# Performance work log

Hardware: AMD Instinct MI355X
Metric: run time of the kernel (lower is better)

## Reference

```python
import jax, jax.numpy as jnp
import numpy as np

L_XYZ = 10  # fourier freqs for position -> 3 + 6*10 = 63 dims
L_DIR = 4   # fourier freqs for direction -> 3 + 6*4 = 27 dims
DIM = 32    # radiance feature dim per depth layer
PPP = 4     # points (depth layers) per pixel
HID = 128   # MLP hidden width
UCH = 64    # UNet hidden channels


def pe(x, L):
    # fourier positional encoding: [x, sin(2^k x), cos(2^k x)]
    f = (2.0 ** jnp.arange(L)).astype(x.dtype)
    xf = x[..., None] * f  # [..., 3, L]
    s = jnp.sin(xf).reshape(x.shape[:-1] + (-1,))
    c = jnp.cos(xf).reshape(x.shape[:-1] + (-1,))
    return jnp.concatenate([x, s, c], axis=-1)


def conv(x, w, b):
    y = jax.lax.conv_general_dilated(x, w, (1, 1), 'SAME',
                                     dimension_numbers=('NCHW', 'OIHW', 'NCHW'))
    return y + b[None, :, None, None]


def setup_inputs() -> dict:
    key = jax.random.key(0)
    ks = jax.random.split(key, 24)
    H = W = 384
    zbufs = jax.random.uniform(ks[0], (H, W, PPP), dtype=jnp.float32)  # depths in [0,1)
    o = jax.random.normal(ks[1], (H, W, 3), dtype=jnp.float32)
    d = jax.random.normal(ks[2], (H, W, 3), dtype=jnp.float32)
    d = d / jnp.linalg.norm(d, axis=-1, keepdims=True)
    cos = jax.random.uniform(ks[3], (H, W, 1), dtype=jnp.float32) * 0.5 + 0.5
    ray = jnp.concatenate([o, d, cos], axis=-1)  # [H,W,7]
    gt = jax.random.uniform(ks[4], (H, W, 3), dtype=jnp.float32)
    mask_gt = jnp.ones((H, W, 1), dtype=jnp.float32)
    xyz_o = jax.random.normal(ks[5], (1024, 3), dtype=jnp.float32)
    in_xyz = 3 + 6 * L_XYZ
    in_dir = 3 + 6 * L_DIR
    in_ch = DIM * PPP
    p = {}
    p['w1'] = jax.random.normal(ks[6], (in_xyz, HID), dtype=jnp.float32) * 0.05
    p['b1'] = jnp.zeros((HID,), dtype=jnp.float32)
    p['w2'] = jax.random.normal(ks[7], (HID, HID), dtype=jnp.float32) * 0.05
    p['b2'] = jnp.zeros((HID,), dtype=jnp.float32)
    p['w3'] = jax.random.normal(ks[8], (HID + in_dir, DIM), dtype=jnp.float32) * 0.05
    p['b3'] = jnp.zeros((DIM,), dtype=jnp.float32)
    p['mpn_w1'] = jax.random.normal(ks[9], (in_ch, in_ch, 3, 3), dtype=jnp.float32) * 0.02
    p['mpn_b1'] = jnp.zeros((in_ch,), dtype=jnp.float32)
    p['mpn_w2'] = jax.random.normal(ks[10], (in_ch, in_ch, 3, 3), dtype=jnp.float32) * 0.02
    p['mpn_b2'] = jnp.zeros((in_ch,), dtype=jnp.float32)
    p['uw1'] = jax.random.normal(ks[11], (UCH, in_ch, 3, 3), dtype=jnp.float32) * 0.02
    p['ub1'] = jnp.zeros((UCH,), dtype=jnp.float32)
    p['uw2'] = jax.random.normal(ks[12], (UCH, UCH, 3, 3), dtype=jnp.float32) * 0.02
    p['ub2'] = jnp.zeros((UCH,), dtype=jnp.float32)
    p['uw3'] = jax.random.normal(ks[13], (3, UCH, 3, 3), dtype=jnp.float32) * 0.02
    p['ub3'] = jnp.zeros((3,), dtype=jnp.float32)
    inp = {'zbufs': zbufs, 'ray': ray, 'gt': gt, 'mask_gt': mask_gt,
           'isTrain': 1, 'xyz_o': xyz_o}
    inp.update(p)
    return inp


def reference(zbufs, ray, gt, mask_gt, isTrain, xyz_o,
              w1, b1, w2, b2, w3, b3,
              mpn_w1, mpn_b1, mpn_w2, mpn_b2,
              uw1, ub1, uw2, ub2, uw3, ub3):
    H, W, P = zbufs.shape
    o = ray[..., :3]
    dirs = ray[..., 3:6]
    cos = ray[..., 6:7]
    thresh = 0.2 if isTrain else 0.0
    # dense equivalent of boolean-mask gather -> MLP -> scatter into zeros
    mask = (zbufs > thresh).astype(zbufs.dtype)  # [H,W,P]
    # xyz_near = o + dirs * zbuf / cos  (xyznear path)
    xyz = o[..., None, :] + dirs[..., None, :] * zbufs[..., None] / cos[..., None]  # [H,W,P,3]
    x = pe(xyz, L_XYZ)                                   # [H,W,P,63]
    h = jax.nn.relu(x @ w1 + b1)                         # [H,W,P,HID]
    h = jax.nn.relu(h @ w2 + b2)
    dpe = pe(dirs, L_DIR)                                # [H,W,27]
    dpe = jnp.broadcast_to(dpe[..., None, :], h.shape[:-1] + (dpe.shape[-1],))
    feat = jnp.concatenate([h, dpe], axis=-1) @ w3 + b3  # [H,W,P,DIM]
    feat = feat * mask[..., None]                        # zeros where pix_mask is False
    # per-layer permute(2,3,0,1) + cat(dim=1) == [1, P*DIM, H, W]
    rdmp = feat.transpose(2, 3, 0, 1).reshape(1, P * DIM, H, W)
    # MPN: predicted per-channel mask
    m = jax.nn.sigmoid(conv(jax.nn.relu(conv(rdmp, mpn_w1, mpn_b1)), mpn_w2, mpn_b2))
    fuse = rdmp * m
    fea_map = jax.nn.sigmoid(fuse[0, :3].transpose(1, 2, 0))  # [H,W,3]
    # UNet refinement to RGB
    u = jax.nn.relu(conv(fuse, uw1, ub1))
    u = jax.nn.relu(conv(u, uw2, ub2))
    img = jax.nn.sigmoid(conv(u, uw3, ub3))[0].transpose(1, 2, 0)  # [H,W,3]
    return img
```

## Files before the change

kernel.cpp:

```cpp
#include <hip/hip_runtime.h>
#include <hip/hip_bf16.h>
#include <math.h>

typedef __attribute__((ext_vector_type(8))) unsigned short ushort8;
typedef __attribute__((ext_vector_type(8))) __bf16 bf16x8;
typedef __attribute__((ext_vector_type(4))) float floatx4;

constexpr int IMGW = 384;
constexpr int NPIX = IMGW * IMGW;

__device__ __forceinline__ unsigned short f2bf(float f) {
  union { float f; unsigned u; } v; v.f = f;
  unsigned u = v.u;
  return (unsigned short)((u + 0x7fffu + ((u >> 16) & 1u)) >> 16);
}
__device__ __forceinline__ float bf2f(unsigned short h) {
  union { unsigned u; float f; } v; v.u = ((unsigned)h) << 16; return v.f;
}
__device__ __forceinline__ unsigned pk2bf(float a, float b) {
  float2 f2; f2.x = a; f2.y = b;
  __hip_bfloat162 h = __float22bfloat162_rn(f2);
  union { __hip_bfloat162 h; unsigned u; } u; u.h = h; return u.u;
}
__device__ __forceinline__ floatx4 mfma16(bf16x8 a, bf16x8 b, floatx4 c) {
  return __builtin_amdgcn_mfma_f32_16x16x32_bf16(a, b, c, 0, 0, 0);
}
__device__ __forceinline__ bf16x8 lds_frag(const unsigned short* p) {
  return *reinterpret_cast<const bf16x8*>(p);
}
__device__ __forceinline__ bf16x8 u4_to_bf(uint4 v) {
  union { uint4 u; bf16x8 b; } c; c.u = v; return c.b;
}

__device__ __forceinline__ void convB_elem(const float* __restrict__ w,
                                           unsigned short* __restrict__ wt,
                                           int i, int CIN, int G, int NT) {
  int j = i & 7, lane = (i >> 3) & 63;
  int rest = i >> 9;
  int nt = rest % NT; int rest2 = rest / NT;
  int g = rest2 % G;  int ks = rest2 / G;
  int q = lane >> 4, m = lane & 15;
  int co = (g * NT + nt) * 16 + m;
  int k = ks * 32 + q * 8 + j;
  int nb = k / CIN, ci = k - nb * CIN;
  wt[i] = f2bf(w[(co * CIN + ci) * 9 + nb]);
}

__global__ __launch_bounds__(256) void prep_all(
    const float* __restrict__ w1, const float* __restrict__ w2, const float* __restrict__ w3,
    const float* __restrict__ mw1, const float* __restrict__ mw2,
    const float* __restrict__ uw1, const float* __restrict__ uw2,
    unsigned short* __restrict__ w1A, unsigned short* __restrict__ w2A,
    unsigned short* __restrict__ w3A,
    unsigned short* __restrict__ cw1, unsigned short* __restrict__ cw2,
    unsigned short* __restrict__ cu1, unsigned short* __restrict__ cu2) {
  int i = blockIdx.x * 256 + threadIdx.x;
  if (i < 28672) {
    if (i < 8192) {
      int j = i & 7, lane = (i >> 3) & 63, t = i >> 9;
      int mt = t >> 1, ks = t & 1;
      int ch_out = mt * 16 + (lane & 15);
      int kp = ks * 32 + (lane >> 4) * 8 + j;
      int chunk = kp >> 3, sl = kp & 7;
      float val;
      if (chunk == 7 && sl >= 4) {
        int c = sl - 4;
        val = (c < 3) ? w1[c * 128 + ch_out] : 0.0f;
      } else {
        const int coordA[8] = {0,0,0,1,1,2,2,2};
        const int octA[8]   = {0,4,8,2,6,0,4,8};
        const int coordB[8] = {0,0,1,1,1,2,2,2};
        const int octB[8]   = {2,6,0,4,8,2,6,0};
        int rc  = (sl < 4) ? coordA[chunk] : coordB[chunk];
        int oct = ((sl < 4) ? octA[chunk] : octB[chunk]) + ((sl >> 1) & 1);
        int korig = ((sl & 1) ? 33 : 3) + rc * 10 + oct;
        val = w1[korig * 128 + ch_out];
      }
      w1A[i] = f2bf(val);
    } else if (i < 24576) {
      int i2 = i - 8192;
      int j = i2 & 7, lane = (i2 >> 3) & 63, t = i2 >> 9;
      int mt = t >> 2, ks = t & 3;
      int ch_out = mt * 16 + (lane & 15);
      int kp = ks * 32 + (lane >> 4) * 8 + j;
      int c_orig = ((kp >> 2) & 7) * 16 + (kp >> 5) * 4 + (kp & 3);
      w2A[i2] = f2bf(w2[c_orig * 128 + ch_out]);
    } else {
      int i3 = i - 24576;
      int j = i3 & 7, lane = (i3 >> 3) & 63, t = i3 >> 9;
      int mt = t >> 2, ks = t & 3;
      int ch_out = mt * 16 + (lane & 15);
      int kp = ks * 32 + (lane >> 4) * 8 + j;
      int c_orig = ((kp >> 2) & 7) * 16 + (kp >> 5) * 4 + (kp & 3);
      w3A[i3] = f2bf(w3[c_orig * 32 + ch_out]);
    }
    return;
  }
  i -= 28672;
  if (i < 147456) { convB_elem(mw1, cw1, i, 128, 4, 2); return; }
  i -= 147456;
  if (i < 147456) { convB_elem(mw2, cw2, i, 128, 4, 2); return; }
  i -= 147456;
  if (i < 73728)  { convB_elem(uw1, cu1, i, 128, 4, 1); return; }
  i -= 73728;
  if (i < 36864)  { convB_elem(uw2, cu2, i, 64, 4, 1); return; }
}

__global__ __launch_bounds__(256) void dcon_kernel(
    const float* __restrict__ ray, const float* __restrict__ w3,
    const float* __restrict__ b3, float* __restrict__ dconG) {
  __shared__ float dpe[8][28];
  int tid = threadIdx.x;
  int pl = tid >> 5, c = tid & 31;
  int pixel = blockIdx.x * 8 + pl;
  const float* r = ray + (size_t)pixel * 7;
  if (c < 3) dpe[pl][c] = r[3 + c];
  if (c < 12) {
    int cc = c >> 2, f = c & 3;
    float s, co;
    __sincosf(r[3 + cc] * (float)(1 << f), &s, &co);
    dpe[pl][3 + cc * 4 + f]  = s;
    dpe[pl][15 + cc * 4 + f] = co;
  }
  __syncthreads();
  float acc = b3[c];
  #pragma unroll
  for (int d = 0; d < 27; ++d)
    acc += dpe[pl][d] * w3[(128 + d) * 32 + c];
  dconG[(size_t)pixel * 32 + c] = acc;
}

__global__ __launch_bounds__(64, 3) void mlp_kernel(
    const float* __restrict__ zbufs, const float* __restrict__ ray,
    const int* __restrict__ isTrain,
    const float* __restrict__ b1, const float* __restrict__ b2,
    const unsigned short* __restrict__ w1A, const unsigned short* __restrict__ w2A,
    const unsigned short* __restrict__ w3A, const float* __restrict__ dconG,
    unsigned short* __restrict__ rdmp, int blk0) {
  __shared__ __align__(16) unsigned short H[64 * 136];

  const int blk = blk0 + blockIdx.x;
  const int lane = threadIdx.x;
  const int q = lane >> 4, m = lane & 15;
  const float thresh = (isTrain[0] != 0) ? 0.2f : 0.0f;

  float fA[2], fB[2];
  int cAi[2], cBi[2];
  #pragma unroll
  for (int half = 0; half < 2; ++half) {
    int ch = half * 4 + q;
    cAi[half] = (ch <= 2) ? 0 : ((ch <= 4) ? 1 : 2);
    fA[half]  = (ch == 0 || ch == 5) ? 1.0f :
                (ch == 1 || ch == 6) ? 16.0f :
                (ch == 2 || ch == 7) ? 256.0f :
                (ch == 3) ? 4.0f : 64.0f;
    cBi[half] = (ch <= 1) ? 0 : ((ch <= 4) ? 1 : 2);
    fB[half]  = (ch == 2) ? 1.0f :
                (ch == 0 || ch == 5) ? 4.0f :
                (ch == 3) ? 16.0f :
                (ch == 1 || ch == 6) ? 64.0f : 256.0f;
  }

  bf16x8 bx[4][2];
  float zs[4];
  #pragma unroll
  for (int nt = 0; nt < 4; ++nt) {
    int s = nt * 16 + m;
    int sg = blk * 64 + s;
    int pixel = sg >> 2;
    float z = zbufs[sg];
    zs[nt] = z;
    const float* r = ray + (size_t)pixel * 7;
    float t = z / r[6];
    float xv0 = r[0] + r[3] * t, xv1 = r[1] + r[4] * t, xv2 = r[2] + r[5] * t;
    #pragma unroll
    for (int half = 0; half < 2; ++half) {
      float uA = (cAi[half] == 0) ? xv0 : ((cAi[half] == 1) ? xv1 : xv2);
      float uB = (cBi[half] == 0) ? xv0 : ((cBi[half] == 1) ? xv1 : xv2);
      float sa, ca, sb, cb;
      __sincosf(uA * fA[half], &sa, &ca);
      __sincosf(uB * fB[half], &sb, &cb);
      float t2a = sa + sa;
      float sa1 = t2a * ca, ca1 = fmaf(-t2a, sa, 1.0f);
      float t2b = sb + sb;
      float sb1 = t2b * cb, cb1 = fmaf(-t2b, sb, 1.0f);
      if (half == 1 && q == 3) { sb = xv0; cb = xv1; sb1 = xv2; cb1 = 0.0f; }
      uint4 dv;
      dv.x = pk2bf(sa, ca); dv.y = pk2bf(sa1, ca1);
      dv.z = pk2bf(sb, cb); dv.w = pk2bf(sb1, cb1);
      bx[nt][half] = u4_to_bf(dv);
    }
  }

  #pragma unroll 1
  for (int half = 0; half < 2; ++half) {
    floatx4 acc[4][4];
    #pragma unroll
    for (int mt = 0; mt < 4; ++mt) {
      float4 bb = *reinterpret_cast<const float4*>(b1 + (half * 4 + mt) * 16 + q * 4);
      #pragma unroll
      for (int nt = 0; nt < 4; ++nt) {
        acc[mt][nt][0] = bb.x; acc[mt][nt][1] = bb.y;
        acc[mt][nt][2] = bb.z; acc[mt][nt][3] = bb.w;
      }
    }
    #pragma unroll
    for (int ks = 0; ks < 2; ++ks) {
      #pragma unroll
      for (int mt = 0; mt < 4; ++mt) {
        int mtg = half * 4 + mt;
        bf16x8 a = *reinterpret_cast<const bf16x8*>(w1A + (((mtg << 1) + ks) << 9) + lane * 8);
        #pragma unroll
        for (int nt = 0; nt < 4; ++nt)
          acc[mt][nt] = mfma16(a, bx[nt][ks], acc[mt][nt]);
      }
    }
    #pragma unroll
    for (int nt = 0; nt < 4; ++nt) {
      uint4* base = reinterpret_cast<uint4*>(&H[(nt * 16 + m) * 136 + q * 32 + half * 16]);
      #pragma unroll
      for (int g = 0; g < 2; ++g) {
        uint4 v;
        v.x = pk2bf(fmaxf(acc[2*g][nt][0], 0.0f),   fmaxf(acc[2*g][nt][1], 0.0f));
        v.y = pk2bf(fmaxf(acc[2*g][nt][2], 0.0f),   fmaxf(acc[2*g][nt][3], 0.0f));
        v.z = pk2bf(fmaxf(acc[2*g+1][nt][0], 0.0f), fmaxf(acc[2*g+1][nt][1], 0.0f));
        v.w = pk2bf(fmaxf(acc[2*g+1][nt][2], 0.0f), fmaxf(acc[2*g+1][nt][3], 0.0f));
        base[g] = v;
      }
    }
  }

  {
    uint4 keep[4][2];
    #pragma unroll 1
    for (int half = 0; half < 2; ++half) {
      floatx4 acc[4][4];
      #pragma unroll
      for (int mt = 0; mt < 4; ++mt) {
        float4 bb = *reinterpret_cast<const float4*>(b2 + (half * 4 + mt) * 16 + q * 4);
        #pragma unroll
        for (int nt = 0; nt < 4; ++nt) {
          acc[mt][nt][0] = bb.x; acc[mt][nt][1] = bb.y;
          acc[mt][nt][2] = bb.z; acc[mt][nt][3] = bb.w;
        }
      }
      bf16x8 acur[4], anxt[4];
      #pragma unroll
      for (int mt = 0; mt < 4; ++mt)
        acur[mt] = *reinterpret_cast<const bf16x8*>(
            w2A + ((((half * 4 + mt) << 2) + 0) << 9) + lane * 8);
      #pragma unroll 1
      for (int ks = 0; ks < 4; ++ks) {
        if (ks + 1 < 4) {
          #pragma unroll
          for (int mt = 0; mt < 4; ++mt)
            anxt[mt] = *reinterpret_cast<const bf16x8*>(
                w2A + ((((half * 4 + mt) << 2) + ks + 1) << 9) + lane * 8);
        }
        bf16x8 bf[4];
        #pragma unroll
        for (int nt = 0; nt < 4; ++nt)
          bf[nt] = lds_frag(H + (nt * 16 + m) * 136 + ks * 32 + q * 8);
        #pragma unroll
        for (int mt = 0; mt < 4; ++mt)
          #pragma unroll
          for (int nt = 0; nt < 4; ++nt)
            acc[mt][nt] = mfma16(acur[mt], bf[nt], acc[mt][nt]);
        #pragma unroll
        for (int mt = 0; mt < 4; ++mt) acur[mt] = anxt[mt];
      }
      #pragma unroll
      for (int nt = 0; nt < 4; ++nt) {
        #pragma unroll
        for (int g = 0; g < 2; ++g) {
          uint4 v;
          v.x = pk2bf(fmaxf(acc[2*g][nt][0], 0.0f),   fmaxf(acc[2*g][nt][1], 0.0f));
          v.y = pk2bf(fmaxf(acc[2*g][nt][2], 0.0f),   fmaxf(acc[2*g][nt][3], 0.0f));
          v.z = pk2bf(fmaxf(acc[2*g+1][nt][0], 0.0f), fmaxf(acc[2*g+1][nt][1], 0.0f));
          v.w = pk2bf(fmaxf(acc[2*g+1][nt][2], 0.0f), fmaxf(acc[2*g+1][nt][3], 0.0f));
          if (half == 0) {
            keep[nt][g] = v;
          } else {
            *reinterpret_cast<uint4*>(&H[(nt * 16 + m) * 136 + q * 32 + 16 + g * 8]) = v;
          }
        }
      }
    }
    #pragma unroll
    for (int nt = 0; nt < 4; ++nt)
      #pragma unroll
      for (int g = 0; g < 2; ++g)
        *reinterpret_cast<uint4*>(&H[(nt * 16 + m) * 136 + q * 32 + g * 8]) = keep[nt][g];
  }

  {
    floatx4 acc[2][4];
    const float* dg = dconG + (size_t)blk * 512;
    #pragma unroll
    for (int nt = 0; nt < 4; ++nt) {
      int s = nt * 16 + m;
      #pragma unroll
      for (int mt = 0; mt < 2; ++mt)
        acc[mt][nt] = *reinterpret_cast<const floatx4*>(dg + (s >> 2) * 32 + mt * 16 + q * 4);
    }
    #pragma unroll
    for (int ks = 0; ks < 4; ++ks) {
      bf16x8 bf[4];
      #pragma unroll
      for (int nt = 0; nt < 4; ++nt)
        bf[nt] = lds_frag(H + (nt * 16 + m) * 136 + ks * 32 + q * 8);
      #pragma unroll
      for (int mt = 0; mt < 2; ++mt) {
        bf16x8 a = *reinterpret_cast<const bf16x8*>(w3A + (((mt << 2) + ks) << 9) + lane * 8);
        #pragma unroll
        for (int nt = 0; nt < 4; ++nt)
          acc[mt][nt] = mfma16(a, bf[nt], acc[mt][nt]);
      }
    }
    #pragma unroll
    for (int nt = 0; nt < 4; ++nt) {
      int s = nt * 16 + m;
      float mk = (zs[nt] > thresh) ? 1.0f : 0.0f;
      unsigned short* dst = rdmp + (size_t)blk * 2048 + s * 32 + q * 4;
      #pragma unroll
      for (int mt = 0; mt < 2; ++mt) {
        uint2 pk;
        pk.x = pk2bf(acc[mt][nt][0] * mk, acc[mt][nt][1] * mk);
        pk.y = pk2bf(acc[mt][nt][2] * mk, acc[mt][nt][3] * mk);
        *reinterpret_cast<uint2*>(dst + mt * 16) = pk;
      }
    }
  }
}

template<int CIN, int COUT, int MODE, int MINW>
__global__ __launch_bounds__(256, MINW) void conv3x3(
    const unsigned short* __restrict__ in, const unsigned short* __restrict__ wt,
    const float* __restrict__ bias, const unsigned short* __restrict__ rdmp,
    unsigned short* __restrict__ out) {
  constexpr int CP  = CIN + 8;
  constexpr int CH8 = CIN / 8;
  constexpr int KC  = CIN / 32;
  constexpr int NT  = COUT / 64;
  constexpr int GROUPS = KC * 3;
  __shared__ __align__(16) unsigned short lds_in[10 * 18 * CP];

  const int tid = threadIdx.x;
  const int x0 = blockIdx.x * 16, y0 = blockIdx.y * 8;

  for (int i = tid; i < 180 * CH8; i += 256) {
    int pix = i / CH8, part = i - pix * CH8;
    int xx = pix % 18, yy = pix / 18;
    int gx = x0 - 1 + xx, gy = y0 - 1 + yy;
    ushort8 v = {0, 0, 0, 0, 0, 0, 0, 0};
    if (gx >= 0 && gx < IMGW && gy >= 0 && gy < IMGW)
      v = *reinterpret_cast<const ushort8*>(in + ((size_t)(gy * IMGW + gx)) * CIN + part * 8);
    *reinterpret_cast<ushort8*>(&lds_in[pix * CP + part * 8]) = v;
  }
  __syncthreads();

  const int wave = tid >> 6, lane = tid & 63, q = lane >> 4, m = lane & 15;
  floatx4 acc[8][NT] = {};

  auto loadB = [&](int g, bf16x8 (&bb)[3][NT]) {
    int kc = g / 3, dx = g - kc * 3;
    #pragma unroll
    for (int dy = 0; dy < 3; ++dy) {
      int ks = (dy * 3 + dx) * KC + kc;
      #pragma unroll
      for (int nt = 0; nt < NT; ++nt)
        bb[dy][nt] = *reinterpret_cast<const bf16x8*>(
            wt + ((((size_t)ks * 4 + wave) * NT + nt) << 9) + lane * 8);
    }
  };

  bf16x8 bcur[3][NT], bnxt[3][NT];
  loadB(0, bcur);

  #pragma unroll 1
  for (int g = 0; g < GROUPS; ++g) {
    if (g + 1 < GROUPS) loadB(g + 1, bnxt);
    int kc = g / 3, dx = g - kc * 3;
    bf16x8 a[10];
    #pragma unroll
    for (int rr = 0; rr < 10; ++rr)
      a[rr] = lds_frag(&lds_in[(rr * 18 + m + dx) * CP + kc * 32 + q * 8]);
    #pragma unroll
    for (int dy = 0; dy < 3; ++dy)
      #pragma unroll
      for (int nt = 0; nt < NT; ++nt)
        #pragma unroll
        for (int mt = 0; mt < 8; ++mt)
          acc[mt][nt] = mfma16(a[mt + dy], bcur[dy][nt], acc[mt][nt]);
    #pragma unroll
    for (int dy = 0; dy < 3; ++dy)
      #pragma unroll
      for (int nt = 0; nt < NT; ++nt)
        bcur[dy][nt] = bnxt[dy][nt];
  }

  const int co0 = wave * (COUT / 4);
  #pragma unroll
  for (int mt = 0; mt < 8; ++mt) {
    int y = y0 + mt;
    #pragma unroll
    for (int nt = 0; nt < NT; ++nt) {
      int co = co0 + nt * 16 + m;
      float bb = bias[co];
      #pragma unroll
      for (int r = 0; r < 4; ++r) {
        int pixel = y * IMGW + x0 + q * 4 + r;
        float v = acc[mt][nt][r] + bb;
        if (MODE == 0) {
          v = fmaxf(v, 0.0f);
        } else {
          v = 1.0f / (1.0f + __expf(-v));
          v *= bf2f(rdmp[(size_t)pixel * 128 + co]);
        }
        out[(size_t)pixel * COUT + co] = f2bf(v);
      }
    }
  }
}

__global__ __launch_bounds__(256) void uconv3_kernel(
    const unsigned short* __restrict__ u2, const float* __restrict__ w,
    const float* __restrict__ b, float* __restrict__ out) {
  __shared__ float wl[1728];
  for (int i = threadIdx.x; i < 1728; i += 256) {
    int c = i % 3; int t = i / 3; int ci = t & 63; int nb = t >> 6;
    wl[i] = w[(c * 64 + ci) * 9 + nb];
  }
  __syncthreads();
  int pixel = blockIdx.x * 256 + threadIdx.x;
  int py = pixel / IMGW, px = pixel - py * IMGW;
  float a0 = b[0], a1 = b[1], a2 = b[2];
  for (int nb = 0; nb < 9; ++nb) {
    int gy = py + nb / 3 - 1, gx = px + nb % 3 - 1;
    if (gx < 0 || gx >= IMGW || gy < 0 || gy >= IMGW) continue;
    const unsigned short* src = u2 + (size_t)(gy * IMGW + gx) * 64;
    const float* wp = wl + nb * 192;
    #pragma unroll
    for (int cc = 0; cc < 8; ++cc) {
      ushort8 v = *reinterpret_cast<const ushort8*>(src + cc * 8);
      #pragma unroll
      for (int j = 0; j < 8; ++j) {
        float uv = bf2f(v[j]);
        const float* w3p = wp + (cc * 8 + j) * 3;
        a0 += uv * w3p[0]; a1 += uv * w3p[1]; a2 += uv * w3p[2];
      }
    }
  }
  float* o = out + (size_t)pixel * 3;
  o[0] = 1.0f / (1.0f + __expf(-a0));
  o[1] = 1.0f / (1.0f + __expf(-a1));
  o[2] = 1.0f / (1.0f + __expf(-a2));
}

extern "C" void kernel_launch(void* const* d_in, const int* in_sizes, int n_in,
                              void* d_out, int out_size, void* d_ws, size_t ws_size,
                              hipStream_t stream) {
  (void)in_sizes; (void)n_in; (void)out_size; (void)ws_size;
  const float* zbufs = (const float*)d_in[0];
  const float* ray   = (const float*)d_in[1];
  const int* isTrain = (const int*)d_in[4];
  const float* w1 = (const float*)d_in[6];
  const float* b1 = (const float*)d_in[7];
  const float* w2 = (const float*)d_in[8];
  const float* b2 = (const float*)d_in[9];
  const float* w3 = (const float*)d_in[10];
  const float* b3 = (const float*)d_in[11];
  const float* mpn_w1 = (const float*)d_in[12];
  const float* mpn_b1 = (const float*)d_in[13];
  const float* mpn_w2 = (const float*)d_in[14];
  const float* mpn_b2 = (const float*)d_in[15];
  const float* uw1 = (const float*)d_in[16];
  const float* ub1 = (const float*)d_in[17];
  const float* uw2 = (const float*)d_in[18];
  const float* ub2 = (const float*)d_in[19];
  const float* uw3 = (const float*)d_in[20];
  const float* ub3 = (const float*)d_in[21];
  float* out = (float*)d_out;

  unsigned char* ws = (unsigned char*)d_ws;
  size_t off = 0;
  auto alloc = [&](size_t bytes) -> void* {
    void* p = ws + off; off = (off + bytes + 255) & ~(size_t)255; return p;
  };
  unsigned short* w1A  = (unsigned short*)alloc(8192 * 2);
  unsigned short* w2A  = (unsigned short*)alloc(16384 * 2);
  unsigned short* w3A  = (unsigned short*)alloc(4096 * 2);
  unsigned short* cw1  = (unsigned short*)alloc((size_t)128 * 1152 * 2);
  unsigned short* cw2  = (unsigned short*)alloc((size_t)128 * 1152 * 2);
  unsigned short* cu1  = (unsigned short*)alloc((size_t)64 * 1152 * 2);
  unsigned short* cu2  = (unsigned short*)alloc((size_t)64 * 576 * 2);
  unsigned short* rdmp = (unsigned short*)alloc((size_t)NPIX * 128 * 2);
  unsigned short* t1   = (unsigned short*)alloc((size_t)NPIX * 128 * 2);
  unsigned short* fuse = (unsigned short*)alloc((size_t)NPIX * 128 * 2);
  unsigned short* u1 = t1;
  unsigned short* u2 = rdmp;
  float* dconG = (float*)fuse;

  prep_all<<<1696, 256, 0, stream>>>(w1, w2, w3, mpn_w1, mpn_w2, uw1, uw2,
                                     w1A, w2A, w3A, cw1, cw2, cu1, cu2);
  dcon_kernel<<<NPIX / 8, 256, 0, stream>>>(ray, w3, b3, dconG);
  const int MLP_BLOCKS = NPIX * 4 / 64;
  mlp_kernel<<<MLP_BLOCKS / 2, 64, 0, stream>>>(zbufs, ray, isTrain, b1, b2,
                                                w1A, w2A, w3A, dconG, rdmp, 0);
  mlp_kernel<<<MLP_BLOCKS / 2, 64, 0, stream>>>(zbufs, ray, isTrain, b1, b2,
                                                w1A, w2A, w3A, dconG, rdmp,
                                                MLP_BLOCKS / 2);

  dim3 cgrid(IMGW / 16, IMGW / 8);
  conv3x3<128, 128, 0, 2><<<cgrid, 256, 0, stream>>>(rdmp, cw1, mpn_b1, nullptr, t1);
  conv3x3<128, 128, 1, 2><<<cgrid, 256, 0, stream>>>(t1, cw2, mpn_b2, rdmp, fuse);
  conv3x3<128, 64, 0, 3><<<cgrid, 256, 0, stream>>>(fuse, cu1, ub1, nullptr, u1);
  conv3x3<64, 64, 0, 3><<<cgrid, 256, 0, stream>>>(u1, cu2, ub2, nullptr, u2);
  uconv3_kernel<<<NPIX / 256, 256, 0, stream>>>(u2, uw3, ub3, out);
}
```

Baseline: 358.3 us.

## Split conv3x3 work across 8 waves by output-channel tile and row group

Conv kernels now launch 512 threads. Each wave owns one 16-wide output-channel tile and a subset of rows, instead of 4 waves each covering all rows and several channel tiles. This shrinks the per-wave accumulator and B-fragment register footprint to raise occupancy and latency hiding. The cost is more LDS A-fragment reads per MFMA, since fragments are no longer shared across channel tiles.

New measurement: 359.1 us. About the same (+0.2%).

```diff
diff --git a/kernel.cpp b/kernel.cpp
--- a/kernel.cpp
+++ b/kernel.cpp
@@ -333,22 +333,24 @@
   }
 }
 
-template<int CIN, int COUT, int MODE, int MINW>
-__global__ __launch_bounds__(256, MINW) void conv3x3(
+template<int CIN, int COUT, int MODE>
+__global__ __launch_bounds__(512, 2) void conv3x3(
     const unsigned short* __restrict__ in, const unsigned short* __restrict__ wt,
     const float* __restrict__ bias, const unsigned short* __restrict__ rdmp,
     unsigned short* __restrict__ out) {
   constexpr int CP  = CIN + 8;
   constexpr int CH8 = CIN / 8;
   constexpr int KC  = CIN / 32;
-  constexpr int NT  = COUT / 64;
   constexpr int GROUPS = KC * 3;
+  constexpr int CS  = COUT / 16;
+  constexpr int YG  = 8 / CS;
+  constexpr int MT  = 8 / YG;
   __shared__ __align__(16) unsigned short lds_in[10 * 18 * CP];
 
   const int tid = threadIdx.x;
   const int x0 = blockIdx.x * 16, y0 = blockIdx.y * 8;
 
-  for (int i = tid; i < 180 * CH8; i += 256) {
+  for (int i = tid; i < 180 * CH8; i += 512) {
     int pix = i / CH8, part = i - pix * CH8;
     int xx = pix % 18, yy = pix / 18;
     int gx = x0 - 1 + xx, gy = y0 - 1 + yy;
@@ -360,65 +362,57 @@
   __syncthreads();
 
   const int wave = tid >> 6, lane = tid & 63, q = lane >> 4, m = lane & 15;
-  floatx4 acc[8][NT] = {};
-
-  auto loadB = [&](int g, bf16x8 (&bb)[3][NT]) {
+  const int cot = wave % CS;
+  const int yb  = (wave / CS) * MT;
+  floatx4 acc[MT] = {};
+
+  auto loadB = [&](int g, bf16x8 (&bb)[3]) {
     int kc = g / 3, dx = g - kc * 3;
     #pragma unroll
     for (int dy = 0; dy < 3; ++dy) {
       int ks = (dy * 3 + dx) * KC + kc;
-      #pragma unroll
-      for (int nt = 0; nt < NT; ++nt)
-        bb[dy][nt] = *reinterpret_cast<const bf16x8*>(
-            wt + ((((size_t)ks * 4 + wave) * NT + nt) << 9) + lane * 8);
+      bb[dy] = *reinterpret_cast<const bf16x8*>(
+          wt + (((size_t)ks * CS + cot) << 9) + lane * 8);
     }
   };
 
-  bf16x8 bcur[3][NT], bnxt[3][NT];
+  bf16x8 bcur[3], bnxt[3];
   loadB(0, bcur);
 
   #pragma unroll 1
   for (int g = 0; g < GROUPS; ++g) {
     if (g + 1 < GROUPS) loadB(g + 1, bnxt);
     int kc = g / 3, dx = g - kc * 3;
-    bf16x8 a[10];
-    #pragma unroll
-    for (int rr = 0; rr < 10; ++rr)
-      a[rr] = lds_frag(&lds_in[(rr * 18 + m + dx) * CP + kc * 32 + q * 8]);
+    bf16x8 a[MT + 2];
+    #pragma unroll
+    for (int rr = 0; rr < MT + 2; ++rr)
+      a[rr] = lds_frag(&lds_in[((yb + rr) * 18 + m + dx) * CP + kc * 32 + q * 8]);
     #pragma unroll
     for (int dy = 0; dy < 3; ++dy)
       #pragma unroll
-      for (int nt = 0; nt < NT; ++nt)
-        #pragma unroll
-        for (int mt = 0; mt < 8; ++mt)
-          acc[mt][nt] = mfma16(a[mt + dy], bcur[dy][nt], acc[mt][nt]);
+      for (int mt = 0; mt < MT; ++mt)
+        acc[mt] = mfma16(a[mt + dy], bcur[dy], acc[mt]);
     #pragma unroll
     for (int dy = 0; dy < 3; ++dy)
-      #pragma unroll
-      for (int nt = 0; nt < NT; ++nt)
-        bcur[dy][nt] = bnxt[dy][nt];
-  }
-
-  const int co0 = wave * (COUT / 4);
+      bcur[dy] = bnxt[dy];
+  }
+
+  const int co = cot * 16 + m;
+  const float bb = bias[co];
   #pragma unroll
-  for (int mt = 0; mt < 8; ++mt) {
-    int y = y0 + mt;
-    #pragma unroll
-    for (int nt = 0; nt < NT; ++nt) {
-      int co = co0 + nt * 16 + m;
-      float bb = bias[co];
-      #pragma unroll
-      for (int r = 0; r < 4; ++r) {
-        int pixel = y * IMGW + x0 + q * 4 + r;
-        float v = acc[mt][nt][r] + bb;
-        if (MODE == 0) {
-          v = fmaxf(v, 0.0f);
-        } else {
-          v = 1.0f / (1.0f + __expf(-v));
-          v *= bf2f(rdmp[(size_t)pixel * 128 + co]);
-        }
-        out[(size_t)pixel * COUT + co] = f2bf(v);
-      }
+  for (int mt = 0; mt < MT; ++mt) {
+    int y = y0 + yb + mt;
+    #pragma unroll
+    for (int r = 0; r < 4; ++r) {
+      int pixel = y * IMGW + x0 + q * 4 + r;
+      float v = acc[mt][r] + bb;
+      if (MODE == 0) {
+        v = fmaxf(v, 0.0f);
+      } else {
+        v = 1.0f / (1.0f + __expf(-v));
+        v *= bf2f(rdmp[(size_t)pixel * 128 + co]);
+      }
+      out[(size_t)pixel * COUT + co] = f2bf(v);
     }
   }
 }
@@ -512,9 +506,9 @@
                                                 MLP_BLOCKS / 2);
 
   dim3 cgrid(IMGW / 16, IMGW / 8);
-  conv3x3<128, 128, 0, 2><<<cgrid, 256, 0, stream>>>(rdmp, cw1, mpn_b1, nullptr, t1);
-  conv3x3<128, 128, 1, 2><<<cgrid, 256, 0, stream>>>(t1, cw2, mpn_b2, rdmp, fuse);
-  conv3x3<128, 64, 0, 3><<<cgrid, 256, 0, stream>>>(fuse, cu1, ub1, nullptr, u1);
-  conv3x3<64, 64, 0, 3><<<cgrid, 256, 0, stream>>>(u1, cu2, ub2, nullptr, u2);
+  conv3x3<128, 128, 0><<<cgrid, 512, 0, stream>>>(rdmp, cw1, mpn_b1, nullptr, t1);
+  conv3x3<128, 128, 1><<<cgrid, 512, 0, stream>>>(t1, cw2, mpn_b2, rdmp, fuse);
+  conv3x3<128, 64, 0><<<cgrid, 512, 0, stream>>>(fuse, cu1, ub1, nullptr, u1);
+  conv3x3<64, 64, 0><<<cgrid, 512, 0, stream>>>(u1, cu2, ub2, nullptr, u2);
   uconv3_kernel<<<NPIX / 256, 256, 0, stream>>>(u2, uw3, ub3, out);
 }
```
